# Kernel tuning notes

Hardware: AMD Instinct MI355X
Metric: run time of the kernel (lower is better)

Reference implementation:

```python
import jax, jax.numpy as jnp
import numpy as np

B, S, D, H, DH, E, DFF = 8, 512, 768, 12, 64, 8, 3072
EPS = 1e-12
SCALE = D ** -0.5  # note: original scales by hidden_size**-0.5, not head_dim


def _ln(x, g, b):
    m = x.mean(-1, keepdims=True)
    v = ((x - m) ** 2).mean(-1, keepdims=True)
    return (x - m) * jax.lax.rsqrt(v + EPS) * g + b


def _expert(x, mask, Wqkv_e, Wd_e, bd_e, g1, be1, W1_e, b1_e, W2_e, b2_e, g2, be2):
    b, s, d = x.shape
    # fused per-head QKV: (B,S,D) x (H,3*DH,D) -> (B,H,S,3*DH)
    qkv = jnp.einsum('bnd,hkd->bhnk', x, Wqkv_e)
    q, k, v = jnp.split(qkv, 3, axis=-1)  # each (B,H,S,DH)
    scores = jnp.einsum('bhid,bhjd->bhij', q, k) * SCALE
    scores = jnp.where(mask[:, None, None, :] == 0, -jnp.inf, scores)
    attn = jax.nn.softmax(scores, axis=-1)
    ctx = jnp.einsum('bhij,bhjd->bhid', attn, v)
    ctx = ctx.transpose(0, 2, 1, 3).reshape(b, s, d)  # concat heads
    att = ctx @ Wd_e.T + bd_e              # attention.dense output (pre-residual)
    feat = att.mean(axis=1)                # (B,D) routing feature (mean over seq)
    h = _ln(att + x, g1, be1)              # post-norm attention block
    ffn = jax.nn.gelu(h @ W1_e.T + b1_e, approximate=False) @ W2_e.T + b2_e
    out = _ln(h + ffn, g2, be2)            # post-norm FFN block (dropout = eval/identity)
    return out, feat


def setup_inputs() -> dict:
    key = jax.random.key(0)
    ks = jax.random.split(key, 8)
    s = 0.02
    return {
        'hidden_states': jax.random.normal(ks[0], (B, S, D), jnp.float32),
        'attention_mask': jnp.ones((B, S), jnp.int32),
        'Wqkv': jax.random.normal(ks[1], (E, H, 3 * DH, D), jnp.float32) * s,
        'Wd': jax.random.normal(ks[2], (E, D, D), jnp.float32) * s,
        'bd': jnp.zeros((E, D), jnp.float32),
        'ln1_g': jnp.ones((E, D), jnp.float32),
        'ln1_b': jnp.zeros((E, D), jnp.float32),
        'W1': jax.random.normal(ks[3], (E, DFF, D), jnp.float32) * s,
        'b1': jnp.zeros((E, DFF), jnp.float32),
        'W2': jax.random.normal(ks[4], (E, D, DFF), jnp.float32) * s,
        'b2': jnp.zeros((E, D), jnp.float32),
        'ln2_g': jnp.ones((E, D), jnp.float32),
        'ln2_b': jnp.zeros((E, D), jnp.float32),
        'centers': jax.random.normal(ks[5], (E, D), jnp.float32) * 0.1,
    }


def reference(hidden_states, attention_mask, Wqkv, Wd, bd, ln1_g, ln1_b,
              W1, b1, W2, b2, ln2_g, ln2_b, centers):
    outs, feats = [], []
    for e in range(centers.shape[0]):  # small fixed set of experts
        o, f = _expert(hidden_states, attention_mask, Wqkv[e], Wd[e], bd[e],
                       ln1_g[e], ln1_b[e], W1[e], b1[e], W2[e], b2[e],
                       ln2_g[e], ln2_b[e])
        outs.append(o)
        feats.append(f)
    outs = jnp.stack(outs)    # (E,B,S,D)
    feats = jnp.stack(feats)  # (E,B,D)
    dists = jnp.linalg.norm(feats - centers[:, None, :], axis=-1)  # (E,B) torch.dist
    sel = jnp.argmin(dists, axis=0)  # (B,) hard routing
    return outs[sel, jnp.arange(outs.shape[1])]  # (B,S,D)
```

## Files before the change

### kernel.cpp

```cpp
#include <hip/hip_runtime.h>
#include <hip/hip_fp16.h>
#include <math.h>
#include <stdint.h>

#define Bb 8
#define Ss 512
#define Dd 768
#define Hh 12
#define Ee 8
#define DFF 3072
#define MROWS 4096
#define QKVN 2304

static __device__ const float SCALE_ = 0.036084391824351615f;

typedef short bf8_t __attribute__((ext_vector_type(8)));
typedef _Float16 f16x4_t __attribute__((ext_vector_type(4)));
typedef float f32x4_t __attribute__((ext_vector_type(4)));

__device__ __forceinline__ float bf2f(unsigned short u){
  union { unsigned int i; float f; } x; x.i = ((unsigned int)u)<<16; return x.f;
}
__device__ __forceinline__ unsigned short f2bf(float f){
  union { float f; unsigned int i; } x; x.f = f;
  unsigned int u = x.i;
  return (unsigned short)((u + 0x7fffu + ((u>>16)&1u)) >> 16);
}

__device__ __forceinline__ void gl_lds16(const void* g, void* l){
  __builtin_amdgcn_global_load_lds(
      (const __attribute__((address_space(1))) unsigned int*)(g),
      (__attribute__((address_space(3))) unsigned int*)(uintptr_t)(l),
      16, 0, 0);
}

__global__ void cast_kernel(const float* __restrict__ in, unsigned short* __restrict__ out, int n){
  int i = (blockIdx.x*256 + threadIdx.x)*4;
  if (i >= n) return;
  const float4 v = *(const float4*)(in + i);
  ushort4 o; o.x=f2bf(v.x); o.y=f2bf(v.y); o.z=f2bf(v.z); o.w=f2bf(v.w);
  *(ushort4*)(out + i) = o;
}

#define VMW6 asm volatile("s_waitcnt vmcnt(6)" ::: "memory")
#define VMW0 asm volatile("s_waitcnt vmcnt(0)" ::: "memory")
#define NOOP ((void)0)

#define STG_A(SL,H,KT) { char* d_ = smem + (SL)*32768 + (H)*16384 + w*1024;          \
    gl_lds16(aSrc[0] + (size_t)(H)*hK + (size_t)(KT)*64, d_);                        \
    gl_lds16(aSrc[1] + (size_t)(H)*hK + (size_t)(KT)*64, d_ + 8192); }
#define STG_B(SL,H,KT) { char* d_ = smem + 65536 + (SL)*32768 + (H)*16384 + w*1024;  \
    gl_lds16(bSrc[0] + (size_t)(H)*hK + (size_t)(KT)*64, d_);                        \
    gl_lds16(bSrc[1] + (size_t)(H)*hK + (size_t)(KT)*64, d_ + 8192); }

#define PHASE(SL, QM, QN, DO_A, STAGE, WAITC)                                        \
  {                                                                                  \
    STAGE;                                                                           \
    WAITC;                                                                           \
    __builtin_amdgcn_s_barrier();                                                    \
    asm volatile("" ::: "memory");                                                   \
    if (DO_A) {                                                                      \
      _Pragma("unroll") for (int i_=0;i_<4;i_++)                                     \
        _Pragma("unroll") for (int k_=0;k_<2;k_++)                                   \
          afr[i_][k_] = *(const bf8_t*)(smem + (SL)*32768 + (QM)*16384 + aoff[i_][k_]); \
    }                                                                                \
    _Pragma("unroll") for (int j_=0;j_<2;j_++)                                       \
      _Pragma("unroll") for (int k_=0;k_<2;k_++)                                     \
        bfr[j_][k_] = *(const bf8_t*)(smem + (SL)*32768 + (QN)*16384 + boff[j_][k_]); \
    asm volatile("s_waitcnt lgkmcnt(0)" ::: "memory");                               \
    __builtin_amdgcn_sched_barrier(0);                                               \
    __builtin_amdgcn_s_setprio(1);                                                   \
    _Pragma("unroll") for (int k_=0;k_<2;k_++)                                       \
      _Pragma("unroll") for (int i_=0;i_<4;i_++)                                     \
        _Pragma("unroll") for (int j_=0;j_<2;j_++)                                   \
          acc[QM][QN][i_][j_] = __builtin_amdgcn_mfma_f32_16x16x32_bf16(             \
              afr[i_][k_], bfr[j_][k_], acc[QM][QN][i_][j_], 0,0,0);                 \
    __builtin_amdgcn_s_setprio(0);                                                   \
    __builtin_amdgcn_s_barrier();                                                    \
  }

__global__ __launch_bounds__(512, 2)
void gemm8p(const unsigned short* __restrict__ A,
            const unsigned short* __restrict__ B,
            unsigned short* __restrict__ C,
            int K, int N, long bStrideZ, long cStrideZ, int swz)
{
  extern __shared__ char smem[];
  const int t = threadIdx.x;
  const int w = t>>6, l = t&63, q4 = l>>4, mr = l&15;
  const int wm = w>>2, wn = w&3;

  int ct, rt, zz;
  if (swz == 1) {
    const int id = (blockIdx.z*gridDim.y + blockIdx.y)*gridDim.x + blockIdx.x;
    const int xcd = id & 7, slot = id >> 3;
    zz = xcd; ct = slot % gridDim.x; rt = slot / gridDim.x;
  } else { ct = blockIdx.x; rt = blockIdx.y; zz = blockIdx.z; }

  const unsigned short* Ap = A + (size_t)rt*256*K;
  const unsigned short* Bp = B + (size_t)zz*bStrideZ + (size_t)ct*256*K;

  const unsigned short* aSrc[2];
  const unsigned short* bSrc[2];
  #pragma unroll
  for (int c=0;c<2;c++){
    const int o  = c*8192 + t*16;
    const int lb = o ^ (((o>>7)&7)<<4);
    const int row = lb>>7, kcol = (lb&127)>>1;
    aSrc[c] = Ap + (size_t)row*K + kcol;
    bSrc[c] = Bp + (size_t)row*K + kcol;
  }
  const size_t hK = (size_t)128*K;

  int aoff[4][2], boff[2][2];
  #pragma unroll
  for (int i=0;i<4;i++)
    #pragma unroll
    for (int kk=0;kk<2;kk++){
      const int row = wm*64 + i*16 + mr;
      int b_ = row*128 + kk*64 + q4*16;
      b_ ^= (row&7)<<4;
      aoff[i][kk] = b_;
    }
  #pragma unroll
  for (int j=0;j<2;j++)
    #pragma unroll
    for (int kk=0;kk<2;kk++){
      const int row = wn*32 + j*16 + mr;
      int b_ = row*128 + kk*64 + q4*16;
      b_ ^= (row&7)<<4;
      boff[j][kk] = 65536 + b_;
    }

  f32x4_t acc[2][2][4][2];
  #pragma unroll
  for (int a0=0;a0<2;a0++)
    #pragma unroll
    for (int a1=0;a1<2;a1++)
      #pragma unroll
      for (int a2=0;a2<4;a2++)
        #pragma unroll
        for (int a3=0;a3<2;a3++) acc[a0][a1][a2][a3] = (f32x4_t){0.f,0.f,0.f,0.f};

  bf8_t afr[4][2], bfr[2][2];

  STG_A(0,0,0); STG_A(0,1,0); STG_B(0,0,0); STG_B(0,1,0);
  STG_A(1,0,1); STG_B(1,1,1);

  const int NITER = K >> 7;
  for (int it = 0; it < NITER-1; ++it){
    const int t1 = 2*it+1, t2 = 2*it+2, t3 = 2*it+3;
    PHASE(0,0,0, 1, STG_A(1,1,t1), VMW6);
    PHASE(0,0,1, 0, STG_B(1,0,t1), NOOP);
    PHASE(0,1,1, 1, STG_A(0,0,t2), NOOP);
    PHASE(0,1,0, 0, STG_B(0,1,t2), NOOP);
    PHASE(1,0,0, 1, STG_A(0,1,t2), VMW6);
    PHASE(1,0,1, 0, STG_B(0,0,t2), NOOP);
    PHASE(1,1,1, 1, STG_A(1,0,t3), NOOP);
    PHASE(1,1,0, 0, STG_B(1,1,t3), NOOP);
  }
  {
    const int t1 = 2*NITER-1;
    PHASE(0,0,0, 1, STG_A(1,1,t1), VMW6);
    PHASE(0,0,1, 0, STG_B(1,0,t1), NOOP);
    PHASE(0,1,1, 1, NOOP, NOOP);
    PHASE(0,1,0, 0, NOOP, NOOP);
    PHASE(1,0,0, 1, NOOP, VMW0);
    PHASE(1,0,1, 0, NOOP, NOOP);
    PHASE(1,1,1, 1, NOOP, NOOP);
    PHASE(1,1,0, 0, NOOP, NOOP);
  }

  unsigned short* Cp = C + (size_t)zz*cStrideZ;
  #pragma unroll
  for (int qm=0;qm<2;qm++)
    #pragma unroll
    for (int qn=0;qn<2;qn++)
      #pragma unroll
      for (int i=0;i<4;i++)
        #pragma unroll
        for (int j=0;j<2;j++){
          const long mb = (long)rt*256 + qm*128 + wm*64 + i*16 + q4*4;
          const long n  = (long)ct*256 + qn*128 + wn*32 + j*16 + mr;
          #pragma unroll
          for (int r=0;r<4;r++)
            Cp[(mb+r)*N + n] = f2bf(acc[qm][qn][i][j][r]);
        }
}

template<int MODE>
__global__ __launch_bounds__(256)
void gemm_bt(const unsigned short* __restrict__ A,
             const unsigned short* __restrict__ Bbf,
             const float* __restrict__ Bf32,
             const float* __restrict__ bias,
             void* __restrict__ Cout,
             int K, int N,
             long bStrideZ, long cStrideZ,
             const int* __restrict__ sel,
             long selAStride, long selBStride, int selBiasStride,
             int swz)
{
  constexpr int BP = (MODE >= 2) ? 40 : 32;
  __shared__ unsigned short As[128*32];
  __shared__ unsigned short Bs[128*BP];

  int rt, ct, zz;
  if (swz == 1) {
    const int id = (blockIdx.z*gridDim.y + blockIdx.y)*gridDim.x + blockIdx.x;
    const int xcd = id & 7, slot = id >> 3;
    zz = xcd; ct = slot % gridDim.x; rt = slot / gridDim.x;
  } else if (swz == 2) {
    const int id = blockIdx.y*gridDim.x + blockIdx.x;
    const int xcd = id & 7, slot = id >> 3;
    rt = xcd*4 + (slot & 3); ct = slot >> 2; zz = 0;
  } else {
    rt = blockIdx.y; ct = blockIdx.x; zz = blockIdx.z;
  }

  const int t = threadIdx.x;
  const int w = t>>6, l = t&63, q4 = l>>4, mr = l&15;
  const int wm = (w&1)*64, wn = (w>>1)*64;
  const int sr = t>>2, cv = t&3;

  const unsigned short* Ap = A;
  const unsigned short* Bp = Bbf;
  const float* Bf_ = Bf32;
  const float* biasp = bias;
  if (MODE == 0) {
    Bp += (size_t)zz * bStrideZ;
  } else {
    const int ex = sel[rt>>2];
    if (MODE == 1) { Ap += (size_t)ex * selAStride; Bp += (size_t)ex * selBStride; }
    else           { Bf_ += (size_t)ex * selBStride; }
    biasp += (long)ex * selBiasStride;
  }

  f32x4_t acc[4][4];
  #pragma unroll
  for (int i=0;i<4;i++)
    #pragma unroll
    for (int j=0;j<4;j++) acc[i][j] = (f32x4_t){0.f,0.f,0.f,0.f};

  const unsigned short* gA = Ap + (size_t)(rt*128 + w*16 + (l>>2))*K + (l&3)*8;
  unsigned short* lA = As + w*512;
  const unsigned short* gB = nullptr;
  unsigned short* lB = Bs + w*512;
  if (MODE < 2) gB = Bp + (size_t)(ct*128 + w*16 + (l>>2))*K + (l&3)*8;

  for (int k0 = 0; k0 < K; k0 += 32) {
    uint4 b0, b1;
    if (MODE >= 2) {
      const float* Br0 = Bf_ + (long)(ct*128 + sr)*K + cv*8 + k0;
      const float* Br1 = Br0 + (long)64*K;
      float4 f0a = *(const float4*)Br0;  float4 f0b = *(const float4*)(Br0+4);
      float4 f1a = *(const float4*)Br1;  float4 f1b = *(const float4*)(Br1+4);
      union { unsigned short s[8]; uint4 v; } p0, p1;
      p0.s[0]=f2bf(f0a.x); p0.s[1]=f2bf(f0a.y); p0.s[2]=f2bf(f0a.z); p0.s[3]=f2bf(f0a.w);
      p0.s[4]=f2bf(f0b.x); p0.s[5]=f2bf(f0b.y); p0.s[6]=f2bf(f0b.z); p0.s[7]=f2bf(f0b.w);
      p1.s[0]=f2bf(f1a.x); p1.s[1]=f2bf(f1a.y); p1.s[2]=f2bf(f1a.z); p1.s[3]=f2bf(f1a.w);
      p1.s[4]=f2bf(f1b.x); p1.s[5]=f2bf(f1b.y); p1.s[6]=f2bf(f1b.z); p1.s[7]=f2bf(f1b.w);
      b0 = p0.v; b1 = p1.v;
    }
    __syncthreads();
    gl_lds16(gA + k0,                lA);
    gl_lds16(gA + (size_t)64*K + k0, lA + 2048);
    if (MODE < 2) {
      gl_lds16(gB + k0,                lB);
      gl_lds16(gB + (size_t)64*K + k0, lB + 2048);
    } else {
      *(uint4*)&Bs[sr*40 + cv*8]      = b0;
      *(uint4*)&Bs[(sr+64)*40 + cv*8] = b1;
    }
    __syncthreads();
    bf8_t af[4], bfv[4];
    #pragma unroll
    for (int i=0;i<4;i++) af[i]  = *(const bf8_t*)&As[(wm+i*16+mr)*32 + q4*8];
    #pragma unroll
    for (int j=0;j<4;j++) bfv[j] = *(const bf8_t*)&Bs[(wn+j*16+mr)*BP + q4*8];
    #pragma unroll
    for (int i=0;i<4;i++)
      #pragma unroll
      for (int j=0;j<4;j++)
        acc[i][j] = __builtin_amdgcn_mfma_f32_16x16x32_bf16(af[i], bfv[j], acc[i][j], 0,0,0);
  }

  const long Cld = N;
  unsigned short* Cb16 = (unsigned short*)Cout + (size_t)zz * cStrideZ;
  float* Cf32 = (float*)Cout;
  #pragma unroll
  for (int j=0;j<4;j++){
    const int n = ct*128 + wn + j*16 + mr;
    const float bv = (MODE==0) ? 0.f : biasp[n];
    #pragma unroll
    for (int i=0;i<4;i++){
      const long mbase = (long)rt*128 + wm + i*16 + q4*4;
      #pragma unroll
      for (int r=0;r<4;r++){
        const float v = acc[i][j][r] + bv;
        const long m = mbase + r;
        if (MODE==0 || MODE==1) {
          Cb16[m*Cld + n] = f2bf(v);
        } else if (MODE==2) {
          const float g = 0.5f*v*(1.0f + erff(v*0.70710678118654752f));
          Cb16[m*Cld + n] = f2bf(g);
        } else {
          Cf32[m*Cld + n] = v;
        }
      }
    }
  }
}

__global__ __launch_bounds__(256)
void attn_kernel(const unsigned short* __restrict__ qkv,
                 const int* __restrict__ mask,
                 unsigned short* __restrict__ ctx,
                 long qkvStrideZ, long ctxStrideZ)
{
  const int qb = blockIdx.x, h = blockIdx.y;
  const int zz = blockIdx.z;
  const int b = zz & 7, e = zz >> 3;
  qkv += (size_t)e * qkvStrideZ;
  ctx += (size_t)e * ctxStrideZ;

  const int t = threadIdx.x, w = t>>6, l = t&63, q4 = l>>4, mr = l&15;
  __shared__ unsigned short Ks[16*72];
  __shared__ unsigned short Vs[64*20];

  const int srow = b*512 + qb*64 + w*16;
  const unsigned short* qp = qkv + (long)(srow+mr)*QKVN + h*192;
  const bf8_t qf0 = *(const bf8_t*)(qp + q4*8);
  const bf8_t qf1 = *(const bf8_t*)(qp + 32 + q4*8);

  f32x4_t cacc[4];
  #pragma unroll
  for (int d=0; d<4; d++) cacc[d] = (f32x4_t){0.f,0.f,0.f,0.f};
  float lsum = 0.f;

  const int el   = t*4;
  const int skey = el>>6;
  const int sd   = el&63;

  for (int kt=0; kt<32; kt++){
    const long krow = (long)(b*512 + kt*16 + skey)*QKVN + h*192;
    const uint2 kv = *(const uint2*)(qkv + krow + 64  + sd);
    const uint2 vv = *(const uint2*)(qkv + krow + 128 + sd);
    __syncthreads();
    *(uint2*)&Ks[skey*72 + sd] = kv;
    {
      const unsigned short* pv = (const unsigned short*)&vv;
      #pragma unroll
      for (int jj=0;jj<4;jj++){
        const __half hv = __float2half(bf2f(pv[jj]));
        Vs[(sd+jj)*20 + skey] = __half_as_ushort(hv);
      }
    }
    __syncthreads();

    const bf8_t kf0 = *(const bf8_t*)&Ks[mr*72 + q4*8];
    const bf8_t kf1 = *(const bf8_t*)&Ks[mr*72 + 32 + q4*8];
    f32x4_t st = __builtin_amdgcn_mfma_f32_16x16x32_bf16(kf0, qf0, (f32x4_t){0.f,0.f,0.f,0.f}, 0,0,0);
    st = __builtin_amdgcn_mfma_f32_16x16x32_bf16(kf1, qf1, st, 0,0,0);

    f16x4_t pf;
    #pragma unroll
    for (int r=0;r<4;r++){
      const int key = kt*16 + q4*4 + r;
      float p = __expf(st[r]*SCALE_);
      if (mask[b*512 + key] == 0) p = 0.f;
      lsum += p;
      pf[r] = (_Float16)p;
    }
    #pragma unroll
    for (int dblk=0; dblk<4; dblk++){
      const f16x4_t vf = *(const f16x4_t*)&Vs[(dblk*16+mr)*20 + q4*4];
      cacc[dblk] = __builtin_amdgcn_mfma_f32_16x16x16f16(pf, vf, cacc[dblk], 0,0,0);
    }
  }

  lsum += __shfl_xor(lsum, 16);
  lsum += __shfl_xor(lsum, 32);
  #pragma unroll
  for (int r=0;r<4;r++){
    const int m2 = q4*4 + r;
    const float lr = __shfl(lsum, m2);
    const float inv = 1.0f/lr;
    const long orow = (long)(b*512 + qb*64 + w*16 + m2)*Dd + h*64;
    #pragma unroll
    for (int dblk=0; dblk<4; dblk++){
      ctx[orow + dblk*16 + mr] = f2bf(cacc[dblk][r]*inv);
    }
  }
}

__global__ void ctxmean_kernel(const unsigned short* __restrict__ ctx, float* __restrict__ out){
  const int d = blockIdx.x*256 + threadIdx.x;
  const int b = blockIdx.y, e = blockIdx.z;
  const unsigned short* p = ctx + ((size_t)e*MROWS + b*512)*Dd + d;
  float s = 0.f;
  for (int i=0;i<512;i++) s += bf2f(p[(size_t)i*Dd]);
  out[((size_t)e*Bb + b)*Dd + d] = s * (1.0f/512.0f);
}

__global__ __launch_bounds__(256)
void featgemm_kernel(const float* __restrict__ ctxmean, const unsigned short* __restrict__ Wdb,
                     const float* __restrict__ bd, float* __restrict__ feat){
  __shared__ float xs[Dd];
  const int b = blockIdx.x, e = blockIdx.y;
  const int t = threadIdx.x;
  for (int i=t;i<Dd;i+=256) xs[i] = ctxmean[((size_t)e*Bb+b)*Dd + i];
  __syncthreads();
  #pragma unroll
  for (int c0=0;c0<3;c0++){
    const int col = c0*256 + t;
    const unsigned short* wr = Wdb + ((size_t)e*Dd + col)*Dd;
    float s = 0.f;
    for (int k=0;k<Dd;k+=8){
      bf8_t wv = *(const bf8_t*)(wr + k);
      const unsigned short* wp = (const unsigned short*)&wv;
      #pragma unroll
      for (int j=0;j<8;j++) s += bf2f(wp[j]) * xs[k+j];
    }
    feat[((size_t)e*Bb+b)*Dd + col] = s + bd[(size_t)e*Dd + col];
  }
}

__global__ void routing_kernel(const float* __restrict__ feat, const float* __restrict__ centers,
                               int* __restrict__ sel)
{
  __shared__ float d2s[64];
  const int t = threadIdx.x;
  if (t < 64){
    const int e = t>>3, b = t&7;
    const float* f = feat + (long)(e*Bb + b)*Dd;
    const float* c = centers + (long)e*Dd;
    float s = 0.f;
    for (int d=0; d<Dd; d++){
      const float df = f[d] - c[d];
      s += df*df;
    }
    d2s[t] = s;
  }
  __syncthreads();
  if (t < 8){
    float best = 3.4e38f; int bi = 0;
    for (int e=0;e<8;e++){ const float v = d2s[e*8+t]; if (v < best){ best=v; bi=e; } }
    sel[t] = bi;
  }
}

__global__ __launch_bounds__(256)
void hprep_kernel(const unsigned short* __restrict__ attsel, const float* __restrict__ x,
                  const float* __restrict__ g, const float* __restrict__ be,
                  const int* __restrict__ sel, unsigned short* __restrict__ hbuf)
{
  const int w = threadIdx.x>>6, l = threadIdx.x&63;
  const int row = blockIdx.x*4 + w;
  const int b = row>>9;
  const int e = sel[b];
  const unsigned short* ap = attsel + (long)row*Dd;
  const float* xp = x + (long)row*Dd;
  float v[12]; float s = 0.f;
  #pragma unroll
  for (int i=0;i<12;i++){ const int d = i*64 + l; v[i] = bf2f(ap[d]) + xp[d]; s += v[i]; }
  #pragma unroll
  for (int o=32;o>0;o>>=1) s += __shfl_xor(s, o);
  const float mean = s * (1.0f/768.0f);
  float vs = 0.f;
  #pragma unroll
  for (int i=0;i<12;i++){ const float dd = v[i]-mean; vs += dd*dd; }
  #pragma unroll
  for (int o=32;o>0;o>>=1) vs += __shfl_xor(vs, o);
  const float rs = rsqrtf(vs*(1.0f/768.0f) + 1e-12f);
  #pragma unroll
  for (int i=0;i<12;i++){
    const int d = i*64 + l;
    hbuf[(long)row*Dd + d] = f2bf((v[i]-mean)*rs*g[(long)e*Dd+d] + be[(long)e*Dd+d]);
  }
}

__global__ __launch_bounds__(256)
void ln2_kernel(const unsigned short* __restrict__ hbuf, const float* __restrict__ tbuf,
                const float* __restrict__ g, const float* __restrict__ be,
                const int* __restrict__ sel, float* __restrict__ out)
{
  const int w = threadIdx.x>>6, l = threadIdx.x&63;
  const int row = blockIdx.x*4 + w;
  const int b = row>>9;
  const int e = sel[b];
  const unsigned short* hp = hbuf + (long)row*Dd;
  const float* tp = tbuf + (long)row*Dd;
  float v[12]; float s = 0.f;
  #pragma unroll
  for (int i=0;i<12;i++){ const int d = i*64 + l; v[i] = bf2f(hp[d]) + tp[d]; s += v[i]; }
  #pragma unroll
  for (int o=32;o>0;o>>=1) s += __shfl_xor(s, o);
  const float mean = s * (1.0f/768.0f);
  float vs = 0.f;
  #pragma unroll
  for (int i=0;i<12;i++){ const float dd = v[i]-mean; vs += dd*dd; }
  #pragma unroll
  for (int o=32;o>0;o>>=1) vs += __shfl_xor(vs, o);
  const float rs = rsqrtf(vs*(1.0f/768.0f) + 1e-12f);
  #pragma unroll
  for (int i=0;i<12;i++){
    const int d = i*64 + l;
    out[(long)row*Dd + d] = (v[i]-mean)*rs*g[(long)e*Dd+d] + be[(long)e*Dd+d];
  }
}

extern "C" void kernel_launch(void* const* d_in, const int* in_sizes, int n_in,
                              void* d_out, int out_size, void* d_ws, size_t ws_size,
                              hipStream_t stream)
{
  const float* x      = (const float*)d_in[0];
  const int*   mask   = (const int*)d_in[1];
  const float* Wqkv   = (const float*)d_in[2];
  const float* Wd     = (const float*)d_in[3];
  const float* bd     = (const float*)d_in[4];
  const float* ln1g   = (const float*)d_in[5];
  const float* ln1b   = (const float*)d_in[6];
  const float* W1     = (const float*)d_in[7];
  const float* b1     = (const float*)d_in[8];
  const float* W2     = (const float*)d_in[9];
  const float* b2     = (const float*)d_in[10];
  const float* ln2g   = (const float*)d_in[11];
  const float* ln2b   = (const float*)d_in[12];
  const float* centers= (const float*)d_in[13];

  hipFuncSetAttribute((const void*)gemm8p, hipFuncAttributeMaxDynamicSharedMemorySize, 131072);

  int zc;
  if      (ws_size >= 258347264ull) zc = 8;
  else if (ws_size >= 182849792ull) zc = 4;
  else if (ws_size >= 145101056ull) zc = 2;
  else                              zc = 1;

  char* p = (char*)d_ws;
  auto carve = [&](size_t bytes)->char*{ char* r = p; p += ((bytes + 255) & ~(size_t)255); return r; };

  unsigned short* xb      = (unsigned short*)carve((size_t)MROWS*Dd*2);
  unsigned short* Wqkvb   = (unsigned short*)carve((size_t)Ee*QKVN*Dd*2);
  unsigned short* Wdb     = (unsigned short*)carve((size_t)Ee*Dd*Dd*2);
  float*          ctxmean = (float*)carve((size_t)Ee*Bb*Dd*4);
  float*          feat    = (float*)carve((size_t)Ee*Bb*Dd*4);
  int*            sel     = (int*)carve(256);
  unsigned short* hbuf    = (unsigned short*)carve((size_t)MROWS*Dd*2);
  unsigned short* attsel  = (unsigned short*)carve((size_t)MROWS*Dd*2);
  unsigned short* qkvchk  = (unsigned short*)carve((size_t)zc*MROWS*QKVN*2);
  unsigned short* ctx_all = (unsigned short*)carve((size_t)Ee*MROWS*Dd*2);
  unsigned short* Gbuf = attsel;
  float*          tbuf = (float*)ctx_all;

  cast_kernel<<<(MROWS*Dd/4 + 255)/256, 256, 0, stream>>>(x, xb, MROWS*Dd);
  cast_kernel<<<(Ee*QKVN*Dd/4 + 255)/256, 256, 0, stream>>>(Wqkv, Wqkvb, Ee*QKVN*Dd);
  cast_kernel<<<(Ee*Dd*Dd/4 + 255)/256, 256, 0, stream>>>(Wd, Wdb, Ee*Dd*Dd);

  const int nchunk = Ee / zc;
  for (int c = 0; c < nchunk; c++){
    gemm8p<<<dim3(QKVN/256, MROWS/256, zc), 512, 131072, stream>>>(
        xb, Wqkvb + (size_t)c*zc*QKVN*Dd, qkvchk,
        Dd, QKVN, (long)QKVN*Dd, (long)MROWS*QKVN, (zc==8) ? 1 : 0);
    attn_kernel<<<dim3(8, Hh, Bb*zc), 256, 0, stream>>>(
        qkvchk, mask, ctx_all + (size_t)c*zc*MROWS*Dd,
        (long)MROWS*QKVN, (long)MROWS*Dd);
    ctxmean_kernel<<<dim3(3, Bb, zc), 256, 0, stream>>>(
        ctx_all + (size_t)c*zc*MROWS*Dd, ctxmean + (size_t)c*zc*Bb*Dd);
  }

  featgemm_kernel<<<dim3(Bb, Ee), 256, 0, stream>>>(ctxmean, Wdb, bd, feat);
  routing_kernel<<<1, 64, 0, stream>>>(feat, centers, sel);

  gemm_bt<1><<<dim3(Dd/128, MROWS/128, 1), 256, 0, stream>>>(
      ctx_all, Wdb, nullptr, bd, attsel, Dd, Dd, 0, 0,
      sel, (long)MROWS*Dd, (long)Dd*Dd, Dd, 2);

  hprep_kernel<<<MROWS/4, 256, 0, stream>>>(attsel, x, ln1g, ln1b, sel, hbuf);
  gemm_bt<2><<<dim3(DFF/128, MROWS/128, 1), 256, 0, stream>>>(
      hbuf, nullptr, W1, b1, Gbuf, Dd, DFF, 0, 0,
      sel, 0, (long)DFF*Dd, DFF, 2);
  gemm_bt<3><<<dim3(Dd/128, MROWS/128, 1), 256, 0, stream>>>(
      Gbuf, nullptr, W2, b2, tbuf, DFF, Dd, 0, 0,
      sel, 0, (long)Dd*DFF, Dd, 2);
  ln2_kernel<<<MROWS/4, 256, 0, stream>>>(hbuf, tbuf, ln2g, ln2b, sel, (float*)d_out);
}
```

Before: 785.6 us.

## Prefetch K/V tiles, cache mask in LDS, use exp2, swizzle attention blocks per XCD

The attention kernel now loads the next K/V tile into registers while the current tile is computed, hiding global load latency behind the MFMA and softmax work. The mask is staged once per block in shared memory as floats and applied by multiplication. The scale is folded into a log2 constant so exp2 can be used. When all experts are processed in one chunk, block IDs are remapped so that blocks sharing the same expert and batch land on the same XCD for better L2 reuse. The costs are extra registers for the prefetch and 2KB of extra LDS per block.

```diff
diff --git a/kernel.cpp b/kernel.cpp
--- a/kernel.cpp
+++ b/kernel.cpp
@@ -13,6 +13,7 @@
 #define QKVN 2304
 
 static __device__ const float SCALE_ = 0.036084391824351615f;
+static __device__ const float SC2_   = 0.05206262648008056f;
 
 typedef short bf8_t __attribute__((ext_vector_type(8)));
 typedef _Float16 f16x4_t __attribute__((ext_vector_type(4)));
@@ -316,17 +317,25 @@
 void attn_kernel(const unsigned short* __restrict__ qkv,
                  const int* __restrict__ mask,
                  unsigned short* __restrict__ ctx,
-                 long qkvStrideZ, long ctxStrideZ)
+                 long qkvStrideZ, long ctxStrideZ, int swz)
 {
-  const int qb = blockIdx.x, h = blockIdx.y;
-  const int zz = blockIdx.z;
+  int qb, h, zz;
+  if (swz) {
+    const int id = (blockIdx.z*gridDim.y + blockIdx.y)*gridDim.x + blockIdx.x;
+    const int xcd = id & 7, slot = id >> 3;
+    const int sz = slot / 96, sxy = slot % 96;
+    qb = sxy & 7; h = sxy >> 3; zz = xcd*8 + sz;
+  } else { qb = blockIdx.x; h = blockIdx.y; zz = blockIdx.z; }
   const int b = zz & 7, e = zz >> 3;
   qkv += (size_t)e * qkvStrideZ;
   ctx += (size_t)e * ctxStrideZ;
 
   const int t = threadIdx.x, w = t>>6, l = t&63, q4 = l>>4, mr = l&15;
+  __shared__ float maskf[512];
   __shared__ unsigned short Ks[16*72];
   __shared__ unsigned short Vs[64*20];
+
+  for (int i=t;i<512;i+=256) maskf[i] = mask[b*512 + i] ? 1.0f : 0.0f;
 
   const int srow = b*512 + qb*64 + w*16;
   const unsigned short* qp = qkv + (long)(srow+mr)*QKVN + h*192;
@@ -341,11 +350,13 @@
   const int el   = t*4;
   const int skey = el>>6;
   const int sd   = el&63;
+  const unsigned short* kbase = qkv + (long)(b*512 + skey)*QKVN + h*192 + 64 + sd;
+  const long kstep = (long)16*QKVN;
+
+  uint2 kv = *(const uint2*)(kbase);
+  uint2 vv = *(const uint2*)(kbase + 64);
 
   for (int kt=0; kt<32; kt++){
-    const long krow = (long)(b*512 + kt*16 + skey)*QKVN + h*192;
-    const uint2 kv = *(const uint2*)(qkv + krow + 64  + sd);
-    const uint2 vv = *(const uint2*)(qkv + krow + 128 + sd);
     __syncthreads();
     *(uint2*)&Ks[skey*72 + sd] = kv;
     {
@@ -356,6 +367,10 @@
         Vs[(sd+jj)*20 + skey] = __half_as_ushort(hv);
       }
     }
+    if (kt < 31){
+      kv = *(const uint2*)(kbase + (long)(kt+1)*kstep);
+      vv = *(const uint2*)(kbase + (long)(kt+1)*kstep + 64);
+    }
     __syncthreads();
 
     const bf8_t kf0 = *(const bf8_t*)&Ks[mr*72 + q4*8];
@@ -363,12 +378,11 @@
     f32x4_t st = __builtin_amdgcn_mfma_f32_16x16x32_bf16(kf0, qf0, (f32x4_t){0.f,0.f,0.f,0.f}, 0,0,0);
     st = __builtin_amdgcn_mfma_f32_16x16x32_bf16(kf1, qf1, st, 0,0,0);
 
+    const f32x4_t mv = *(const f32x4_t*)&maskf[kt*16 + q4*4];
     f16x4_t pf;
     #pragma unroll
     for (int r=0;r<4;r++){
-      const int key = kt*16 + q4*4 + r;
-      float p = __expf(st[r]*SCALE_);
-      if (mask[b*512 + key] == 0) p = 0.f;
+      const float p = __builtin_exp2f(st[r]*SC2_) * mv[r];
       lsum += p;
       pf[r] = (_Float16)p;
     }
@@ -564,7 +578,7 @@
         Dd, QKVN, (long)QKVN*Dd, (long)MROWS*QKVN, (zc==8) ? 1 : 0);
     attn_kernel<<<dim3(8, Hh, Bb*zc), 256, 0, stream>>>(
         qkvchk, mask, ctx_all + (size_t)c*zc*MROWS*Dd,
-        (long)MROWS*QKVN, (long)MROWS*Dd);
+        (long)MROWS*QKVN, (long)MROWS*Dd, (zc==8) ? 1 : 0);
     ctxmean_kernel<<<dim3(3, Bb, zc), 256, 0, stream>>>(
         ctx_all + (size_t)c*zc*MROWS*Dd, ctxmean + (size_t)c*zc*Bb*Dd);
   }
```

Result: no change. 781.9 us (-0.5%).
